# Kernel tuning notes

Hardware: AMD Instinct MI355X
Metric: run time of the kernel (lower is better)

## Reference

```python
import jax, jax.numpy as jnp
import numpy as np

N = 50000
E = 800000
D = 128   # input_dim
O = 128   # output_dim


def setup_inputs() -> dict:
    key = jax.random.key(0)
    ks = jax.random.split(key, 12)
    s = 0.05
    inp = {
        "x": jax.random.normal(ks[0], (N, D), dtype=jnp.float32),
        "edge_index": jax.random.randint(ks[1], (2, E), 0, N, dtype=jnp.int64),
        # lin_src_to_dst / lin_dst_to_src
        "w_s2d": jax.random.normal(ks[2], (D, O), dtype=jnp.float32) * s,
        "b_s2d": jnp.zeros((O,), dtype=jnp.float32),
        "w_d2s": jax.random.normal(ks[3], (D, O), dtype=jnp.float32) * s,
        "b_d2s": jnp.zeros((O,), dtype=jnp.float32),
        # edge_mlp: Linear(2D -> D), ReLU, Linear(D -> 1)
        "w_e1": jax.random.normal(ks[4], (2 * D, D), dtype=jnp.float32) * s,
        "b_e1": jnp.zeros((D,), dtype=jnp.float32),
        "w_e2": jax.random.normal(ks[5], (D, 1), dtype=jnp.float32) * s,
        "b_e2": jnp.zeros((1,), dtype=jnp.float32),
        # gate_mlp: Linear(2O -> O), ReLU, Linear(O -> 1)
        "w_g1": jax.random.normal(ks[6], (2 * O, O), dtype=jnp.float32) * s,
        "b_g1": jnp.zeros((O,), dtype=jnp.float32),
        "w_g2": jax.random.normal(ks[7], (O, 1), dtype=jnp.float32) * s,
        "b_g2": jnp.zeros((1,), dtype=jnp.float32),
    }
    return inp


def reference(x, edge_index, w_s2d, b_s2d, w_d2s, b_d2s,
              w_e1, b_e1, w_e2, b_e2, w_g1, b_g1, w_g2, b_g2):
    num_nodes = x.shape[0]
    src = edge_index[0]
    dst = edge_index[1]

    x_src = x[src]                      # [E, D]
    x_dst = x[dst]                      # [E, D]

    # edge-wise contribution score a_ij in (0,1)
    edge_input = jnp.concatenate([x_src, x_dst], axis=-1)          # [E, 2D]
    h_e = jax.nn.relu(edge_input @ w_e1 + b_e1)                    # [E, D]
    edge_score = jax.nn.sigmoid((h_e @ w_e2 + b_e2)[:, 0])         # [E]

    # directional messages, scaled by edge score
    msg_in = (x_src @ w_s2d + b_s2d) * edge_score[:, None]         # [E, O]
    msg_out = (x_dst @ w_d2s + b_d2s) * edge_score[:, None]        # [E, O]

    # scatter-add to nodes
    h_in = jax.ops.segment_sum(msg_in, dst, num_segments=num_nodes)   # [N, O]
    h_out = jax.ops.segment_sum(msg_out, src, num_segments=num_nodes) # [N, O]

    # degree normalization (clamped at 1)
    ones = jnp.ones((src.shape[0],), dtype=x.dtype)
    in_deg = jnp.maximum(jax.ops.segment_sum(ones, dst, num_segments=num_nodes), 1.0)
    out_deg = jnp.maximum(jax.ops.segment_sum(ones, src, num_segments=num_nodes), 1.0)
    h_in = h_in / in_deg[:, None]
    h_out = h_out / out_deg[:, None]

    # node-wise gate fusing the two directions
    gate_input = jnp.concatenate([h_in, h_out], axis=-1)           # [N, 2O]
    h_g = jax.nn.relu(gate_input @ w_g1 + b_g1)                    # [N, O]
    g = jax.nn.sigmoid(h_g @ w_g2 + b_g2)                          # [N, 1]

    fused = g * h_in + (1.0 - g) * h_out                           # [N, O]
    # input_dim == output_dim -> residual is Identity
    return fused + x
```

## Files before the change

kernel.cpp:

```cpp
#include <hip/hip_runtime.h>

#define N_NODES 50000
#define N_EDGES 800000
#define NBKT 391
#define BKT 128
#define MAXREC 2560
#define EPB 4096
#define XCBLK 6250

typedef unsigned int u32;
typedef unsigned short u16;
typedef __attribute__((ext_vector_type(2))) float float2v;
typedef __attribute__((ext_vector_type(8))) short bf16x8;
typedef __attribute__((ext_vector_type(4))) float f32x4;

__device__ __forceinline__ float bf_lo(u32 v){ return __uint_as_float(v << 16); }
__device__ __forceinline__ float bf_hi(u32 v){ return __uint_as_float(v & 0xffff0000u); }
__device__ __forceinline__ u16 f2bf(float f){
    u32 u = __float_as_uint(f);
    u += 0x7fffu + ((u >> 16) & 1u);
    return (u16)(u >> 16);
}

#if __has_builtin(__builtin_amdgcn_cvt_pk_f32_fp8) && __has_builtin(__builtin_amdgcn_cvt_pk_fp8_f32)
#define HW_FP8 1
#else
#define HW_FP8 0
#endif

__device__ __forceinline__ u32 enc1_e4m3(float f){
    u32 u = __float_as_uint(f);
    u32 s = (u >> 24) & 0x80u;
    u32 a = u & 0x7fffffffu;
    if (a >= 0x43e00000u) return s | 0x7eu;
    if (a < 0x3c800000u){
        float af = __uint_as_float(a) * 512.f;
        u32 m = (u32)(af + 0.5f);
        return s | m;
    }
    int e = (int)(a >> 23) - 127;
    u32 mant = (a >> 20) & 7u;
    u32 rnd = (a >> 19) & 1u;
    u32 sticky = (a & 0x7ffffu) ? 1u : 0u;
    u32 code = ((u32)(e + 7) << 3) | mant;
    code += (rnd & (sticky | (mant & 1u)));
    if (code > 0x7eu) code = 0x7eu;
    return s | code;
}

template<bool HI>
__device__ __forceinline__ float2v dec2_word(u32 v){
#if HW_FP8
    return __builtin_amdgcn_cvt_pk_f32_fp8(v, HI);
#else
    u32 v16 = HI ? (v >> 16) : (v & 0xffffu);
    float2v r;
    #pragma unroll
    for (int t = 0; t < 2; t++){
        u32 b = (v16 >> (8 * t)) & 0xffu;
        u32 e = (b >> 3) & 15u, m = b & 7u;
        float fv = e ? __uint_as_float(((e + 120u) << 23) | (m << 20)) : (float)m * 0.001953125f;
        r[t] = (b & 0x80u) ? -fv : fv;
    }
    return r;
#endif
}
__device__ __forceinline__ u32 encpk_lo(float a, float b, u32 old){
#if HW_FP8
    return (u32)__builtin_amdgcn_cvt_pk_fp8_f32(a, b, (int)old, false);
#else
    return (old & 0xffff0000u) | enc1_e4m3(a) | (enc1_e4m3(b) << 8);
#endif
}
__device__ __forceinline__ u32 encpk_hi(float a, float b, u32 old){
#if HW_FP8
    return (u32)__builtin_amdgcn_cvt_pk_fp8_f32(a, b, (int)old, true);
#else
    return (old & 0x0000ffffu) | (enc1_e4m3(a) << 16) | (enc1_e4m3(b) << 24);
#endif
}

__global__ __launch_bounds__(256) void setup_kernel(const float* __restrict__ x,
        const float* __restrict__ w_s2d, const float* __restrict__ w_d2s,
        const float* __restrict__ w_e1, const float* __restrict__ w_g1,
        const float* __restrict__ b_e1,
        uint2* __restrict__ xb2, u32* __restrict__ xf8,
        u16* __restrict__ pk1, u16* __restrict__ pkM,
        u16* __restrict__ pkG, float* __restrict__ bias1, u32* __restrict__ bcnt){
    const int blk = blockIdx.x, tid = threadIdx.x;
    if (blk < XCBLK){
        int i = blk * 256 + tid;
        float4 v = ((const float4*)x)[i];
        uint2 o;
        o.x = (u32)f2bf(v.x) | ((u32)f2bf(v.y) << 16);
        o.y = (u32)f2bf(v.z) | ((u32)f2bf(v.w) << 16);
        xb2[i] = o;
        u32 w8 = encpk_lo(v.x, v.y, 0u);
        xf8[i] = encpk_hi(v.z, v.w, w8);
    } else if (blk < XCBLK + 386){
        int idx = (blk - XCBLK) * 256 + tid;
        if (idx < 32768){
            int j = idx & 7, g = (idx >> 3) & 3, ch = (idx >> 5) & 255, ks = idx >> 13;
            int k = ks * 32 + g * 8 + j;
            float v = (ch < 128) ? w_e1[k * 128 + ch] : w_e1[(128 + k) * 128 + (ch - 128)];
            pk1[idx] = f2bf(v);
        } else if (idx < 65536){
            int i2 = idx - 32768;
            int j = i2 & 7, g = (i2 >> 3) & 3, ch = (i2 >> 5) & 255, ks = i2 >> 13;
            int k = ks * 32 + g * 8 + j;
            float v = (ch < 128) ? w_s2d[k * 128 + ch] : w_d2s[k * 128 + (ch - 128)];
            pkM[i2] = f2bf(v);
        } else if (idx < 98304){
            int i2 = idx - 65536;
            int j = i2 & 7, g = (i2 >> 3) & 3, oc = (i2 >> 5) & 127, ks = i2 >> 12;
            int k = ks * 32 + g * 8 + j;
            pkG[i2] = f2bf(w_g1[k * 128 + oc]);
        } else if (idx < 98560){
            int o = idx - 98304;
            bias1[o] = (o < 128) ? b_e1[o] : 0.f;
        }
    } else {
        for (int i = tid; i < 2 * NBKT; i += 256) bcnt[i] = 0u;
    }
}

__global__ __launch_bounds__(256) void proj_mfma_kernel(const u16* __restrict__ xb16,
        const u16* __restrict__ pk1, const float* __restrict__ bias1, u32* __restrict__ T1){
    const int tid = threadIdx.x;
    const int w = tid >> 6, l = tid & 63;
    const int l16 = l & 15, lg = l >> 4;
    const int n0 = blockIdx.x * 16;
    const int node = n0 + l16;
    bf16x8 bx[4];
    #pragma unroll
    for (int ks = 0; ks < 4; ks++)
        bx[ks] = *(const bf16x8*)(xb16 + node * 128 + ks * 32 + lg * 8);
    #pragma unroll
    for (int ct = 0; ct < 4; ct++){
        const int ch0 = w * 64 + ct * 16;
        f32x4 acc = {0.f, 0.f, 0.f, 0.f};
        #pragma unroll
        for (int ks = 0; ks < 4; ks++){
            bf16x8 a = *(const bf16x8*)(pk1 + ((ks * 256 + ch0 + l16) * 4 + lg) * 8);
            acc = __builtin_amdgcn_mfma_f32_16x16x32_bf16(a, bx[ks], acc, 0, 0, 0);
        }
        const int chb = ch0 + lg * 4;
        float f0 = acc[0] + bias1[chb],     f1 = acc[1] + bias1[chb + 1];
        float f2 = acc[2] + bias1[chb + 2], f3 = acc[3] + bias1[chb + 3];
        u32 wd = encpk_lo(f0, f1, 0u);
        wd = encpk_hi(f2, f3, wd);
        T1[node * 64 + (chb >> 2)] = wd;
    }
}

__global__ __launch_bounds__(256) void edge_score_kernel(const u32* __restrict__ T1w, const int* __restrict__ eidx,
        const float* __restrict__ w_e2, const float* __restrict__ b_e2,
        u16* __restrict__ score){
    const int l16 = threadIdx.x & 15;
    const int e = blockIdx.x * 16 + (threadIdx.x >> 4);
    const int src = eidx[e];
    const int dst = eidx[N_EDGES + e];
    const uint2 a8 = *(const uint2*)(T1w + src * 64 + l16 * 2);
    const uint2 b8 = *(const uint2*)(T1w + dst * 64 + 32 + l16 * 2);
    float2v a0 = dec2_word<false>(a8.x), a1 = dec2_word<true>(a8.x);
    float2v a2 = dec2_word<false>(a8.y), a3 = dec2_word<true>(a8.y);
    float2v b0 = dec2_word<false>(b8.x), b1 = dec2_word<true>(b8.x);
    float2v b2 = dec2_word<false>(b8.y), b3 = dec2_word<true>(b8.y);
    const float4 w0 = ((const float4*)w_e2)[l16 * 2];
    const float4 w1 = ((const float4*)w_e2)[l16 * 2 + 1];
    float p = fmaxf(a0[0] + b0[0], 0.f) * w0.x + fmaxf(a0[1] + b0[1], 0.f) * w0.y
            + fmaxf(a1[0] + b1[0], 0.f) * w0.z + fmaxf(a1[1] + b1[1], 0.f) * w0.w
            + fmaxf(a2[0] + b2[0], 0.f) * w1.x + fmaxf(a2[1] + b2[1], 0.f) * w1.y
            + fmaxf(a3[0] + b3[0], 0.f) * w1.z + fmaxf(a3[1] + b3[1], 0.f) * w1.w;
    p += __shfl_xor(p, 1, 64);
    p += __shfl_xor(p, 2, 64);
    p += __shfl_xor(p, 4, 64);
    p += __shfl_xor(p, 8, 64);
    if (l16 == 0){
        float sc = 1.f / (1.f + __expf(-(p + b_e2[0])));
        score[e] = f2bf(sc);
    }
}

__global__ __launch_bounds__(256) void count_kernel(const int* __restrict__ eidx, u32* __restrict__ bcnt){
    __shared__ u32 h[2 * NBKT];
    const int tid = threadIdx.x;
    for (int i = tid; i < 2 * NBKT; i += 256) h[i] = 0u;
    __syncthreads();
    const int e0 = blockIdx.x * EPB;
    for (int i = tid; i < EPB; i += 256){
        int e = e0 + i;
        if (e < N_EDGES){
            atomicAdd(&h[eidx[N_EDGES + e] >> 7], 1u);
            atomicAdd(&h[NBKT + (eidx[e] >> 7)], 1u);
        }
    }
    __syncthreads();
    for (int i = tid; i < 2 * NBKT; i += 256){
        u32 v = h[i];
        if (v) atomicAdd(&bcnt[i], v);
    }
}

__global__ __launch_bounds__(512) void bucket_scan_kernel(const u32* __restrict__ bcnt,
        u32* __restrict__ bbase, u32* __restrict__ bnext){
    __shared__ u32 sa[512], sb[512];
    const int t = threadIdx.x;
    const u32* c = bcnt + blockIdx.x * NBKT;
    u32* base = bbase + blockIdx.x * (NBKT + 1);
    u32* nxt  = bnext + blockIdx.x * NBKT;
    sa[t] = (t < NBKT) ? c[t] : 0u;
    __syncthreads();
    u32 *a = sa, *b = sb;
    for (int off = 1; off < 512; off <<= 1){
        u32 v = a[t]; if (t >= off) v += a[t - off];
        b[t] = v; __syncthreads();
        u32* tmp = a; a = b; b = tmp;
    }
    if (t < NBKT){
        u32 ex = t ? a[t - 1] : 0u;
        base[t] = ex; nxt[t] = ex;
        if (t == NBKT - 1) base[NBKT] = a[t];
    }
}

__global__ __launch_bounds__(256) void bucket1_kernel(const int* __restrict__ eidx, const u16* __restrict__ score,
        u32* __restrict__ bnext, uint2* __restrict__ Bd, uint2* __restrict__ Bs){
    __shared__ u32 hd[NBKT], hs[NBKT];
    __shared__ u32 rbd[NBKT], rbs[NBKT];
    __shared__ u32 ld[NBKT], ls[NBKT];
    const int tid = threadIdx.x;
    for (int i = tid; i < NBKT; i += 256){ hd[i] = 0u; hs[i] = 0u; ld[i] = 0u; ls[i] = 0u; }
    __syncthreads();
    const int e0 = blockIdx.x * EPB;
    for (int i = tid; i < EPB; i += 256){
        int e = e0 + i;
        if (e < N_EDGES){
            atomicAdd(&hd[eidx[N_EDGES + e] >> 7], 1u);
            atomicAdd(&hs[eidx[e] >> 7], 1u);
        }
    }
    __syncthreads();
    for (int i = tid; i < NBKT; i += 256){
        rbd[i] = hd[i] ? atomicAdd(&bnext[i], hd[i]) : 0u;
        rbs[i] = hs[i] ? atomicAdd(&bnext[NBKT + i], hs[i]) : 0u;
    }
    __syncthreads();
    for (int i = tid; i < EPB; i += 256){
        int e = e0 + i;
        if (e < N_EDGES){
            int src = eidx[e], dst = eidx[N_EDGES + e];
            u32 sc = (u32)score[e] << 16;
            int bd = dst >> 7;
            u32 r = atomicAdd(&ld[bd], 1u);
            Bd[rbd[bd] + r] = make_uint2(sc | (u32)src, (u32)(dst & 127));
            int bs_ = src >> 7;
            u32 r2 = atomicAdd(&ls[bs_], 1u);
            Bs[rbs[bs_] + r2] = make_uint2(sc | (u32)dst, (u32)(src & 127));
        }
    }
}

__global__ __launch_bounds__(256) void bucket2_kernel(const uint2* __restrict__ Bd, const uint2* __restrict__ Bs,
        const u32* __restrict__ bbase,
        u32* __restrict__ cnt_dst, u32* __restrict__ start_dst,
        u32* __restrict__ cnt_src, u32* __restrict__ start_src,
        u32* __restrict__ in_pay, u32* __restrict__ out_pay){
    __shared__ u32 pays[MAXREC];
    __shared__ u16 locs[MAXREC];
    __shared__ u32 hist[BKT], nxt[BKT], pref[BKT];
    const int tid = threadIdx.x;
    const int side = blockIdx.x >= NBKT ? 1 : 0;
    const int b = side ? blockIdx.x - NBKT : blockIdx.x;
    const uint2* __restrict__ B = side ? Bs : Bd;
    const u32* bb = bbase + side * (NBKT + 1);
    const u32 base = bb[b];
    const u32 nrec = bb[b + 1] - base;
    u32* cnto = side ? cnt_src : cnt_dst;
    u32* sto  = side ? start_src : start_dst;
    u32* payo = side ? out_pay : in_pay;
    for (int i = tid; i < BKT; i += 256) hist[i] = 0u;
    __syncthreads();
    for (u32 i = tid; i < nrec; i += 256){
        uint2 r = B[base + i];
        if (i < MAXREC){ pays[i] = r.x; locs[i] = (u16)r.y; }
        atomicAdd(&hist[r.y & (BKT - 1)], 1u);
    }
    __syncthreads();
    if (tid < BKT) pref[tid] = hist[tid];
    __syncthreads();
    for (int off = 1; off < BKT; off <<= 1){
        u32 v = 0;
        if (tid < BKT){ v = pref[tid]; if (tid >= off) v += pref[tid - off]; }
        __syncthreads();
        if (tid < BKT) pref[tid] = v;
        __syncthreads();
    }
    if (tid < BKT){
        u32 ex = tid ? pref[tid - 1] : 0u;
        u32 gstart = base + ex;
        nxt[tid] = gstart;
        int node = b * BKT + tid;
        if (node < N_NODES){ cnto[node] = hist[tid]; sto[node] = gstart; }
    }
    __syncthreads();
    for (u32 i = tid; i < nrec; i += 256){
        u32 pay; int loc;
        if (i < MAXREC){ pay = pays[i]; loc = locs[i]; }
        else { uint2 r = B[base + i]; pay = r.x; loc = (int)(r.y & (BKT - 1)); }
        u32 pos = atomicAdd(&nxt[loc], 1u);
        payo[pos] = pay;
    }
}

__global__ __launch_bounds__(256) void gather_kernel(const u32* __restrict__ xf8,
        const u32* __restrict__ in_pay, const u32* __restrict__ out_pay,
        const u32* __restrict__ cnt_dst, const u32* __restrict__ start_dst,
        const u32* __restrict__ cnt_src, const u32* __restrict__ start_src,
        u32* __restrict__ Y, float* __restrict__ ssin, float* __restrict__ ssout){
    const int w = threadIdx.x >> 6, lane = threadIdx.x & 63;
    const int node = blockIdx.x * 2 + (w >> 1);
    const int dir = w & 1;
    const u32* __restrict__ pay = dir ? out_pay : in_pay;
    const u32 deg = dir ? cnt_src[node] : cnt_dst[node];
    const u32 st  = dir ? start_src[node] : start_dst[node];
    const int half = lane >> 5, l5 = lane & 31;
    float a0 = 0.f, a1 = 0.f, a2 = 0.f, a3 = 0.f, ss = 0.f;
    u32 j = (u32)half;
    for (; j + 6 < deg; j += 8){
        u32 p0 = pay[st+j], p1 = pay[st+j+2], p2 = pay[st+j+4], p3 = pay[st+j+6];
        u32 v0 = xf8[(p0 & 0xffffu)*32 + l5], v1 = xf8[(p1 & 0xffffu)*32 + l5];
        u32 v2 = xf8[(p2 & 0xffffu)*32 + l5], v3 = xf8[(p3 & 0xffffu)*32 + l5];
        float s0 = __uint_as_float(p0 & 0xffff0000u), s1 = __uint_as_float(p1 & 0xffff0000u);
        float s2 = __uint_as_float(p2 & 0xffff0000u), s3 = __uint_as_float(p3 & 0xffff0000u);
        float2v e0l = dec2_word<false>(v0), e0h = dec2_word<true>(v0);
        float2v e1l = dec2_word<false>(v1), e1h = dec2_word<true>(v1);
        float2v e2l = dec2_word<false>(v2), e2h = dec2_word<true>(v2);
        float2v e3l = dec2_word<false>(v3), e3h = dec2_word<true>(v3);
        a0 += s0*e0l[0] + s1*e1l[0] + s2*e2l[0] + s3*e3l[0];
        a1 += s0*e0l[1] + s1*e1l[1] + s2*e2l[1] + s3*e3l[1];
        a2 += s0*e0h[0] + s1*e1h[0] + s2*e2h[0] + s3*e3h[0];
        a3 += s0*e0h[1] + s1*e1h[1] + s2*e2h[1] + s3*e3h[1];
        ss += s0 + s1 + s2 + s3;
    }
    for (; j < deg; j += 2){
        u32 pl = pay[st + j];
        u32 v = xf8[(pl & 0xffffu)*32 + l5];
        float sc = __uint_as_float(pl & 0xffff0000u);
        float2v el = dec2_word<false>(v), eh = dec2_word<true>(v);
        a0 += sc * el[0]; a1 += sc * el[1];
        a2 += sc * eh[0]; a3 += sc * eh[1];
        ss += sc;
    }
    a0 += __shfl_xor(a0, 32, 64);
    a1 += __shfl_xor(a1, 32, 64);
    a2 += __shfl_xor(a2, 32, 64);
    a3 += __shfl_xor(a3, 32, 64);
    ss += __shfl_xor(ss, 32, 64);
    if (half == 0){
        uint2 o;
        o.x = (u32)f2bf(a0) | ((u32)f2bf(a1) << 16);
        o.y = (u32)f2bf(a2) | ((u32)f2bf(a3) << 16);
        *(uint2*)(Y + node * 128 + dir * 64 + l5 * 2) = o;
    }
    if (lane == 0){
        if (dir) ssout[node] = ss; else ssin[node] = ss;
    }
}

__global__ __launch_bounds__(256) void finale_mfma_kernel(const u32* __restrict__ Yw,
        const float* __restrict__ x,
        const u16* __restrict__ pkM, const u16* __restrict__ pkG,
        const float* __restrict__ b_s2d, const float* __restrict__ b_d2s,
        const float* __restrict__ ssin, const float* __restrict__ ssout,
        const u32* __restrict__ cnt_dst, const u32* __restrict__ cnt_src,
        const float* __restrict__ b_g1, const float* __restrict__ w_g2, const float* __restrict__ b_g2,
        float* __restrict__ out){
    __shared__ u32 Hsh[16][132];
    __shared__ float part[16][17];
    __shared__ float gl[16];
    const int tid = threadIdx.x;
    const int w = tid >> 6, l = tid & 63;
    const int l16 = l & 15, lg = l >> 4;
    const int n0 = blockIdx.x * 16;
    const int node = n0 + l16;
    const int dir = w >> 1;
    const int cb = (w & 1) * 64;
    const u16* Yh = (const u16*)Yw;
    bf16x8 yf[4];
    #pragma unroll
    for (int ks = 0; ks < 4; ks++)
        yf[ks] = *(const bf16x8*)(Yh + node * 256 + dir * 128 + ks * 32 + lg * 8);
    const float ssv  = dir ? ssout[node] : ssin[node];
    const float dinv = 1.f / fmaxf((float)(dir ? cnt_src[node] : cnt_dst[node]), 1.f);
    const float* bv = dir ? b_d2s : b_s2d;
    #pragma unroll
    for (int ct = 0; ct < 4; ct++){
        const int chl = cb + ct * 16;
        f32x4 acc = {0.f, 0.f, 0.f, 0.f};
        #pragma unroll
        for (int ks = 0; ks < 4; ks++){
            bf16x8 a = *(const bf16x8*)(pkM + ((ks * 256 + dir * 128 + chl + l16) * 4 + lg) * 8);
            acc = __builtin_amdgcn_mfma_f32_16x16x32_bf16(a, yf[ks], acc, 0, 0, 0);
        }
        const int chb = chl + lg * 4;
        float h0 = (acc[0] + ssv * bv[chb])     * dinv;
        float h1 = (acc[1] + ssv * bv[chb + 1]) * dinv;
        float h2 = (acc[2] + ssv * bv[chb + 2]) * dinv;
        float h3 = (acc[3] + ssv * bv[chb + 3]) * dinv;
        const int wi = (dir * 128 + chb) >> 1;
        Hsh[l16][wi]     = (u32)f2bf(h0) | ((u32)f2bf(h1) << 16);
        Hsh[l16][wi + 1] = (u32)f2bf(h2) | ((u32)f2bf(h3) << 16);
    }
    __syncthreads();
    bf16x8 hb[8];
    #pragma unroll
    for (int ks = 0; ks < 8; ks++)
        hb[ks] = *(const bf16x8*)((const u16*)&Hsh[l16][0] + ks * 32 + lg * 8);
    float p = 0.f;
    #pragma unroll
    for (int ct2 = 0; ct2 < 2; ct2++){
        const int oc0 = w * 32 + ct2 * 16;
        f32x4 acc = {0.f, 0.f, 0.f, 0.f};
        #pragma unroll
        for (int ks = 0; ks < 8; ks++){
            bf16x8 a = *(const bf16x8*)(pkG + ((ks * 128 + oc0 + l16) * 4 + lg) * 8);
            acc = __builtin_amdgcn_mfma_f32_16x16x32_bf16(a, hb[ks], acc, 0, 0, 0);
        }
        const int ob = oc0 + lg * 4;
        #pragma unroll
        for (int r = 0; r < 4; r++)
            p += fmaxf(acc[r] + b_g1[ob + r], 0.f) * w_g2[ob + r];
    }
    part[l16][w * 4 + lg] = p;
    __syncthreads();
    if (tid < 16){
        float s = 0.f;
        #pragma unroll
        for (int i = 0; i < 16; i++) s += part[tid][i];
        gl[tid] = 1.f / (1.f + __expf(-(s + b_g2[0])));
    }
    __syncthreads();
    {
        const int nn = tid >> 4, o = (tid & 15) * 8;
        const float gv = gl[nn];
        const int gbase = (n0 + nn) * 128 + o;
        float4 x0 = *(const float4*)(x + gbase);
        float4 x1 = *(const float4*)(x + gbase + 4);
        float r[8];
        #pragma unroll
        for (int t = 0; t < 4; t++){
            u32 hi = Hsh[nn][(o >> 1) + t];
            u32 ho = Hsh[nn][64 + (o >> 1) + t];
            r[2*t]   = gv * bf_lo(hi) + (1.f - gv) * bf_lo(ho);
            r[2*t+1] = gv * bf_hi(hi) + (1.f - gv) * bf_hi(ho);
        }
        *(float4*)(out + gbase)     = make_float4(r[0]+x0.x, r[1]+x0.y, r[2]+x0.z, r[3]+x0.w);
        *(float4*)(out + gbase + 4) = make_float4(r[4]+x1.x, r[5]+x1.y, r[6]+x1.z, r[7]+x1.w);
    }
}

extern "C" void kernel_launch(void* const* d_in, const int* in_sizes, int n_in,
                              void* d_out, int out_size, void* d_ws, size_t ws_size,
                              hipStream_t stream){
    const float* x     = (const float*)d_in[0];
    const int*   ei    = (const int*)d_in[1];
    const float* w_s2d = (const float*)d_in[2];
    const float* b_s2d = (const float*)d_in[3];
    const float* w_d2s = (const float*)d_in[4];
    const float* b_d2s = (const float*)d_in[5];
    const float* w_e1  = (const float*)d_in[6];
    const float* b_e1  = (const float*)d_in[7];
    const float* w_e2  = (const float*)d_in[8];
    const float* b_e2  = (const float*)d_in[9];
    const float* w_g1  = (const float*)d_in[10];
    const float* b_g1  = (const float*)d_in[11];
    const float* w_g2  = (const float*)d_in[12];
    const float* b_g2  = (const float*)d_in[13];
    float* out = (float*)d_out;
    u32*   T1  = (u32*)d_out;
    uint2* Bd  = (uint2*)d_out;
    uint2* Bs  = Bd + N_EDGES;
    u32*   Y   = (u32*)d_out;

    char* ws = (char*)d_ws;
    size_t off = 0;
    #define TAKE(name, bytes) char* name = ws + off; off += (((size_t)(bytes)) + 511) & ~(size_t)511;
    TAKE(pk1_b,   32768 * 2)
    TAKE(pkM_b,   32768 * 2)
    TAKE(pkG_b,   32768 * 2)
    TAKE(bias1_b, 256 * 4)
    TAKE(xb_b,    (size_t)N_NODES * 128 * 2)
    TAKE(xf8_b,   (size_t)N_NODES * 128)
    TAKE(score_b, (size_t)N_EDGES * 2)
    TAKE(bcnt_b,  (size_t)2 * NBKT * 4)
    TAKE(bbase_b, (size_t)2 * (NBKT + 1) * 4)
    TAKE(bnext_b, (size_t)2 * NBKT * 4)
    TAKE(cnt_b,   (size_t)2 * N_NODES * 4)
    TAKE(sd_b,    (size_t)N_NODES * 4)
    TAKE(ss2_b,   (size_t)N_NODES * 4)
    TAKE(ipay_b,  (size_t)N_EDGES * 4)
    TAKE(opay_b,  (size_t)N_EDGES * 4)
    TAKE(ssin_b,  (size_t)N_NODES * 4)
    TAKE(ssout_b, (size_t)N_NODES * 4)
    #undef TAKE
    (void)ws_size; (void)in_sizes; (void)n_in; (void)out_size;

    setup_kernel<<<XCBLK + 386 + 1, 256, 0, stream>>>(x, w_s2d, w_d2s, w_e1, w_g1, b_e1,
        (uint2*)xb_b, (u32*)xf8_b, (u16*)pk1_b, (u16*)pkM_b, (u16*)pkG_b,
        (float*)bias1_b, (u32*)bcnt_b);
    count_kernel<<<(N_EDGES + EPB - 1) / EPB, 256, 0, stream>>>(ei, (u32*)bcnt_b);
    proj_mfma_kernel<<<N_NODES / 16, 256, 0, stream>>>((const u16*)xb_b,
        (const u16*)pk1_b, (const float*)bias1_b, T1);
    edge_score_kernel<<<N_EDGES / 16, 256, 0, stream>>>((const u32*)T1, ei, w_e2, b_e2,
        (u16*)score_b);
    bucket_scan_kernel<<<2, 512, 0, stream>>>((const u32*)bcnt_b, (u32*)bbase_b, (u32*)bnext_b);
    bucket1_kernel<<<(N_EDGES + EPB - 1) / EPB, 256, 0, stream>>>(ei, (const u16*)score_b,
        (u32*)bnext_b, Bd, Bs);
    bucket2_kernel<<<2 * NBKT, 256, 0, stream>>>(Bd, Bs, (const u32*)bbase_b,
        (u32*)cnt_b, (u32*)sd_b, (u32*)cnt_b + N_NODES, (u32*)ss2_b,
        (u32*)ipay_b, (u32*)opay_b);
    gather_kernel<<<N_NODES / 2, 256, 0, stream>>>((const u32*)xf8_b,
        (const u32*)ipay_b, (const u32*)opay_b,
        (const u32*)cnt_b, (const u32*)sd_b, (const u32*)cnt_b + N_NODES, (const u32*)ss2_b,
        Y, (float*)ssin_b, (float*)ssout_b);
    finale_mfma_kernel<<<N_NODES / 16, 256, 0, stream>>>((const u32*)Y, x,
        (const u16*)pkM_b, (const u16*)pkG_b, b_s2d, b_d2s,
        (const float*)ssin_b, (const float*)ssout_b,
        (const u32*)cnt_b, (const u32*)cnt_b + N_NODES,
        b_g1, w_g2, b_g2, out);
}
```

Before: 224.2 us.

## Fuse bucket counting into setup kernel and vectorize edge-score and gather math

Moves the per-bucket edge histogram (count_kernel) into extra blocks of setup_kernel, with a hipMemsetAsync clearing the global counters beforehand. This removes one kernel launch and lets the counting overlap with the x conversion work. It also rewrites the edge-score dot product and the gather accumulation with float2 vector operations, which may let the compiler emit packed FP32 instructions. The memset adds a separate stream operation, and the float2 rewrite changes the order of floating-point summation.

```diff
diff --git a/kernel.cpp b/kernel.cpp
--- a/kernel.cpp
+++ b/kernel.cpp
@@ -7,6 +7,7 @@
 #define MAXREC 2560
 #define EPB 4096
 #define XCBLK 6250
+#define CNTBLK 196
 
 typedef unsigned int u32;
 typedef unsigned short u16;
@@ -83,7 +84,7 @@
 __global__ __launch_bounds__(256) void setup_kernel(const float* __restrict__ x,
         const float* __restrict__ w_s2d, const float* __restrict__ w_d2s,
         const float* __restrict__ w_e1, const float* __restrict__ w_g1,
-        const float* __restrict__ b_e1,
+        const float* __restrict__ b_e1, const int* __restrict__ eidx,
         uint2* __restrict__ xb2, u32* __restrict__ xf8,
         u16* __restrict__ pk1, u16* __restrict__ pkM,
         u16* __restrict__ pkG, float* __restrict__ bias1, u32* __restrict__ bcnt){
@@ -120,7 +121,22 @@
             bias1[o] = (o < 128) ? b_e1[o] : 0.f;
         }
     } else {
-        for (int i = tid; i < 2 * NBKT; i += 256) bcnt[i] = 0u;
+        __shared__ u32 h[2 * NBKT];
+        for (int i = tid; i < 2 * NBKT; i += 256) h[i] = 0u;
+        __syncthreads();
+        const int e0 = (blk - XCBLK - 386) * EPB;
+        for (int i = tid; i < EPB; i += 256){
+            int e = e0 + i;
+            if (e < N_EDGES){
+                atomicAdd(&h[eidx[N_EDGES + e] >> 7], 1u);
+                atomicAdd(&h[NBKT + (eidx[e] >> 7)], 1u);
+            }
+        }
+        __syncthreads();
+        for (int i = tid; i < 2 * NBKT; i += 256){
+            u32 v = h[i];
+            if (v) atomicAdd(&bcnt[i], v);
+        }
     }
 }
 
@@ -162,16 +178,24 @@
     const int dst = eidx[N_EDGES + e];
     const uint2 a8 = *(const uint2*)(T1w + src * 64 + l16 * 2);
     const uint2 b8 = *(const uint2*)(T1w + dst * 64 + 32 + l16 * 2);
-    float2v a0 = dec2_word<false>(a8.x), a1 = dec2_word<true>(a8.x);
-    float2v a2 = dec2_word<false>(a8.y), a3 = dec2_word<true>(a8.y);
-    float2v b0 = dec2_word<false>(b8.x), b1 = dec2_word<true>(b8.x);
-    float2v b2 = dec2_word<false>(b8.y), b3 = dec2_word<true>(b8.y);
-    const float4 w0 = ((const float4*)w_e2)[l16 * 2];
-    const float4 w1 = ((const float4*)w_e2)[l16 * 2 + 1];
-    float p = fmaxf(a0[0] + b0[0], 0.f) * w0.x + fmaxf(a0[1] + b0[1], 0.f) * w0.y
-            + fmaxf(a1[0] + b1[0], 0.f) * w0.z + fmaxf(a1[1] + b1[1], 0.f) * w0.w
-            + fmaxf(a2[0] + b2[0], 0.f) * w1.x + fmaxf(a2[1] + b2[1], 0.f) * w1.y
-            + fmaxf(a3[0] + b3[0], 0.f) * w1.z + fmaxf(a3[1] + b3[1], 0.f) * w1.w;
+    const float2v* wv = (const float2v*)(w_e2 + l16 * 8);
+    const float2v zero = {0.f, 0.f};
+    float2v acc = {0.f, 0.f};
+    {
+        float2v t0 = dec2_word<false>(a8.x) + dec2_word<false>(b8.x);
+        float2v t1 = dec2_word<true>(a8.x)  + dec2_word<true>(b8.x);
+        float2v t2 = dec2_word<false>(a8.y) + dec2_word<false>(b8.y);
+        float2v t3 = dec2_word<true>(a8.y)  + dec2_word<true>(b8.y);
+        t0 = __builtin_elementwise_max(t0, zero);
+        t1 = __builtin_elementwise_max(t1, zero);
+        t2 = __builtin_elementwise_max(t2, zero);
+        t3 = __builtin_elementwise_max(t3, zero);
+        acc += t0 * wv[0];
+        acc += t1 * wv[1];
+        acc += t2 * wv[2];
+        acc += t3 * wv[3];
+    }
+    float p = acc[0] + acc[1];
     p += __shfl_xor(p, 1, 64);
     p += __shfl_xor(p, 2, 64);
     p += __shfl_xor(p, 4, 64);
@@ -179,26 +203,6 @@
     if (l16 == 0){
         float sc = 1.f / (1.f + __expf(-(p + b_e2[0])));
         score[e] = f2bf(sc);
-    }
-}
-
-__global__ __launch_bounds__(256) void count_kernel(const int* __restrict__ eidx, u32* __restrict__ bcnt){
-    __shared__ u32 h[2 * NBKT];
-    const int tid = threadIdx.x;
-    for (int i = tid; i < 2 * NBKT; i += 256) h[i] = 0u;
-    __syncthreads();
-    const int e0 = blockIdx.x * EPB;
-    for (int i = tid; i < EPB; i += 256){
-        int e = e0 + i;
-        if (e < N_EDGES){
-            atomicAdd(&h[eidx[N_EDGES + e] >> 7], 1u);
-            atomicAdd(&h[NBKT + (eidx[e] >> 7)], 1u);
-        }
-    }
-    __syncthreads();
-    for (int i = tid; i < 2 * NBKT; i += 256){
-        u32 v = h[i];
-        if (v) atomicAdd(&bcnt[i], v);
     }
 }
 
@@ -325,7 +329,8 @@
     const u32 deg = dir ? cnt_src[node] : cnt_dst[node];
     const u32 st  = dir ? start_src[node] : start_dst[node];
     const int half = lane >> 5, l5 = lane & 31;
-    float a0 = 0.f, a1 = 0.f, a2 = 0.f, a3 = 0.f, ss = 0.f;
+    float2v AL = {0.f, 0.f}, AH = {0.f, 0.f};
+    float ss = 0.f;
     u32 j = (u32)half;
     for (; j + 6 < deg; j += 8){
         u32 p0 = pay[st+j], p1 = pay[st+j+2], p2 = pay[st+j+4], p3 = pay[st+j+6];
@@ -333,25 +338,21 @@
         u32 v2 = xf8[(p2 & 0xffffu)*32 + l5], v3 = xf8[(p3 & 0xffffu)*32 + l5];
         float s0 = __uint_as_float(p0 & 0xffff0000u), s1 = __uint_as_float(p1 & 0xffff0000u);
         float s2 = __uint_as_float(p2 & 0xffff0000u), s3 = __uint_as_float(p3 & 0xffff0000u);
-        float2v e0l = dec2_word<false>(v0), e0h = dec2_word<true>(v0);
-        float2v e1l = dec2_word<false>(v1), e1h = dec2_word<true>(v1);
-        float2v e2l = dec2_word<false>(v2), e2h = dec2_word<true>(v2);
-        float2v e3l = dec2_word<false>(v3), e3h = dec2_word<true>(v3);
-        a0 += s0*e0l[0] + s1*e1l[0] + s2*e2l[0] + s3*e3l[0];
-        a1 += s0*e0l[1] + s1*e1l[1] + s2*e2l[1] + s3*e3l[1];
-        a2 += s0*e0h[0] + s1*e1h[0] + s2*e2h[0] + s3*e3h[0];
-        a3 += s0*e0h[1] + s1*e1h[1] + s2*e2h[1] + s3*e3h[1];
+        AL += dec2_word<false>(v0) * s0;  AH += dec2_word<true>(v0) * s0;
+        AL += dec2_word<false>(v1) * s1;  AH += dec2_word<true>(v1) * s1;
+        AL += dec2_word<false>(v2) * s2;  AH += dec2_word<true>(v2) * s2;
+        AL += dec2_word<false>(v3) * s3;  AH += dec2_word<true>(v3) * s3;
         ss += s0 + s1 + s2 + s3;
     }
     for (; j < deg; j += 2){
         u32 pl = pay[st + j];
         u32 v = xf8[(pl & 0xffffu)*32 + l5];
         float sc = __uint_as_float(pl & 0xffff0000u);
-        float2v el = dec2_word<false>(v), eh = dec2_word<true>(v);
-        a0 += sc * el[0]; a1 += sc * el[1];
-        a2 += sc * eh[0]; a3 += sc * eh[1];
+        AL += dec2_word<false>(v) * sc;
+        AH += dec2_word<true>(v) * sc;
         ss += sc;
     }
+    float a0 = AL[0], a1 = AL[1], a2 = AH[0], a3 = AH[1];
     a0 += __shfl_xor(a0, 32, 64);
     a1 += __shfl_xor(a1, 32, 64);
     a2 += __shfl_xor(a2, 32, 64);
@@ -506,10 +507,10 @@
     #undef TAKE
     (void)ws_size; (void)in_sizes; (void)n_in; (void)out_size;
 
-    setup_kernel<<<XCBLK + 386 + 1, 256, 0, stream>>>(x, w_s2d, w_d2s, w_e1, w_g1, b_e1,
+    hipMemsetAsync(bcnt_b, 0, (size_t)2 * NBKT * 4, stream);
+    setup_kernel<<<XCBLK + 386 + CNTBLK, 256, 0, stream>>>(x, w_s2d, w_d2s, w_e1, w_g1, b_e1, ei,
         (uint2*)xb_b, (u32*)xf8_b, (u16*)pk1_b, (u16*)pkM_b, (u16*)pkG_b,
         (float*)bias1_b, (u32*)bcnt_b);
-    count_kernel<<<(N_EDGES + EPB - 1) / EPB, 256, 0, stream>>>(ei, (u32*)bcnt_b);
     proj_mfma_kernel<<<N_NODES / 16, 256, 0, stream>>>((const u16*)xb_b,
         (const u16*)pk1_b, (const float*)bias1_b, T1);
     edge_score_kernel<<<N_EDGES / 16, 256, 0, stream>>>((const u32*)T1, ei, w_e2, b_e2,
```

After: 228.8 us. 1.02x slower.
